# Kernel optimization log

Measured on AMD Instinct MI355X. Metric: run time of the kernel, lower is better.

Reference implementation:

```python
import jax, jax.numpy as jnp
import numpy as np

HEADS = 8


def setup_inputs() -> dict:
    key = jax.random.key(0)
    k1, k2, k3, k4, k5, k6 = jax.random.split(key, 6)
    B, S, E = 2, 2048, 512
    D = E // HEADS
    return {
        "values": jax.random.normal(k1, (B, S, E), dtype=jnp.float32),
        "keys": jax.random.normal(k2, (B, S, E), dtype=jnp.float32),
        "queries": jax.random.normal(k3, (B, S, E), dtype=jnp.float32),
        "mask": jax.random.randint(k4, (B, 1, 1, S), 0, 2, dtype=jnp.int32),
        "W_v": jax.random.normal(k5, (D, D), dtype=jnp.float32) * (1.0 / np.sqrt(D)),
        "W_o": jax.random.normal(k6, (E, E), dtype=jnp.float32) * (1.0 / np.sqrt(E)),
        "b_o": jnp.zeros((E,), dtype=jnp.float32),
    }


def reference(values, keys, queries, mask, W_v, W_o, b_o):
    B, S, E = queries.shape
    H = HEADS
    D = E // H
    # reshape to (b, s, h, d) and apply the SAME W_v linear to v, k, q
    # (faithful to the original, which calls self.values on all three)
    v = jnp.einsum('bshd,ed->bshe', values.reshape(B, -1, H, D), W_v)
    k = jnp.einsum('bshd,ed->bshe', keys.reshape(B, -1, H, D), W_v)
    q = jnp.einsum('bshd,ed->bshe', queries.reshape(B, -1, H, D), W_v)
    # unscaled attention scores (original has no 1/sqrt(d))
    energy = jnp.einsum('bqhd,bkhd->bhqk', q, k)  # (b, h, q, k)
    energy = jnp.where(mask == 0, -jnp.inf, energy)
    attn = jax.nn.softmax(energy, axis=3)
    out = jnp.einsum('bhqk,bkhd->bqhd', attn, v)  # (b, q, h, d)
    out = out.reshape(B, S, E)
    return out @ W_o.T + b_o
```

## Files before the change

kernel.cpp:

```cpp
#include <hip/hip_runtime.h>


#define B_ 2
#define S_ 2048
#define E_ 512
#define H_ 8
#define D_ 64

typedef unsigned short ushort_t;
typedef __attribute__((ext_vector_type(8))) short short8;
typedef __attribute__((ext_vector_type(8))) _Float16 half8;
typedef __attribute__((ext_vector_type(4))) float f32x4;

__device__ __forceinline__ ushort_t f2bs(float x) {
    union { float f; unsigned int u; } a; a.f = x;
    unsigned int u = a.u;
    u += 0x7fffu + ((u >> 16) & 1u);
    return (ushort_t)(u >> 16);
}
__device__ __forceinline__ float bs2f(ushort_t h) {
    union { unsigned int u; float f; } a; a.u = ((unsigned int)h) << 16;
    return a.f;
}
__device__ __forceinline__ ushort_t f2hs(float x) {
    _Float16 h = (_Float16)x;
    ushort_t u; __builtin_memcpy(&u, &h, 2);
    return u;
}
__device__ __forceinline__ void split16(const float4* g, ushort_t* hi, ushort_t* lo) {
    #pragma unroll
    for (int q = 0; q < 4; ++q) {
        float4 f = g[q];
        float vv[4] = {f.x, f.y, f.z, f.w};
        #pragma unroll
        for (int j = 0; j < 4; ++j) {
            ushort_t h = f2bs(vv[j]);
            hi[q * 4 + j] = h;
            lo[q * 4 + j] = f2bs(vv[j] - bs2f(h));
        }
    }
}

__global__ void __launch_bounds__(256) proj_mfma(
    const float* __restrict__ quer, const float* __restrict__ keys,
    const float* __restrict__ vals, const float* __restrict__ Wv,
    ushort_t* __restrict__ qf, ushort_t* __restrict__ kf,
    ushort_t* __restrict__ vt)
{
    __shared__ ushort_t Ah[64 * 72], Al[64 * 72];
    __shared__ ushort_t Bh[64 * 72], Bl[64 * 72];
    const int tens = blockIdx.y;
    const float* src = tens == 0 ? quer : (tens == 1 ? keys : vals);
    const int bx = blockIdx.x;
    const int st = bx & 31, bh = bx >> 5;
    const int b = bh >> 3, h = bh & 7;
    const int s0 = st * 64;
    const int t = threadIdx.x;

    {
        int e = t >> 2, dg = (t & 3) * 16;
        ushort_t th[16], tl[16];
        split16((const float4*)(Wv + e * 64 + dg), th, tl);
        *(uint4*)&Bh[e * 72 + dg] = *(uint4*)th;  *(uint4*)&Bh[e * 72 + dg + 8] = *(uint4*)(th + 8);
        *(uint4*)&Bl[e * 72 + dg] = *(uint4*)tl;  *(uint4*)&Bl[e * 72 + dg + 8] = *(uint4*)(tl + 8);
    }
    {
        int row = t >> 2, cg = (t & 3) * 16;
        const float* g = src + ((size_t)b * S_ + s0 + row) * 512 + h * 64 + cg;
        ushort_t th[16], tl[16];
        split16((const float4*)g, th, tl);
        *(uint4*)&Ah[row * 72 + cg] = *(uint4*)th;  *(uint4*)&Ah[row * 72 + cg + 8] = *(uint4*)(th + 8);
        *(uint4*)&Al[row * 72 + cg] = *(uint4*)tl;  *(uint4*)&Al[row * 72 + cg + 8] = *(uint4*)(tl + 8);
    }
    __syncthreads();

    const int w = t >> 6, lm = t & 15, quad = (t >> 4) & 3;
    f32x4 acc[4];
    #pragma unroll
    for (int nt = 0; nt < 4; ++nt) acc[nt] = (f32x4){0.f, 0.f, 0.f, 0.f};

    #pragma unroll
    for (int kk = 0; kk < 2; ++kk) {
        short8 ah = *(const short8*)&Ah[(w * 16 + lm) * 72 + kk * 32 + quad * 8];
        short8 al = *(const short8*)&Al[(w * 16 + lm) * 72 + kk * 32 + quad * 8];
        #pragma unroll
        for (int nt = 0; nt < 4; ++nt) {
            short8 bh8 = *(const short8*)&Bh[(nt * 16 + lm) * 72 + kk * 32 + quad * 8];
            short8 bl8 = *(const short8*)&Bl[(nt * 16 + lm) * 72 + kk * 32 + quad * 8];
            acc[nt] = __builtin_amdgcn_mfma_f32_16x16x32_bf16(ah, bh8, acc[nt], 0, 0, 0);
            acc[nt] = __builtin_amdgcn_mfma_f32_16x16x32_bf16(al, bh8, acc[nt], 0, 0, 0);
            acc[nt] = __builtin_amdgcn_mfma_f32_16x16x32_bf16(ah, bl8, acc[nt], 0, 0, 0);
        }
    }

    if (tens < 2) {
        ushort_t* dst = tens == 0 ? qf : kf;
        #pragma unroll
        for (int nt = 0; nt < 4; ++nt) {
            #pragma unroll
            for (int r = 0; r < 4; ++r) {
                size_t addr = ((size_t)bh * S_ + s0 + w * 16 + quad * 4 + r) * 64 + nt * 16 + lm;
                dst[addr] = f2hs(acc[nt][r]);
            }
        }
    } else {
        #pragma unroll
        for (int nt = 0; nt < 4; ++nt) {
            unsigned int p0 = (unsigned int)f2bs(acc[nt][0]) | ((unsigned int)f2bs(acc[nt][1]) << 16);
            unsigned int p1 = (unsigned int)f2bs(acc[nt][2]) | ((unsigned int)f2bs(acc[nt][3]) << 16);
            uint2 pk; pk.x = p0; pk.y = p1;
            size_t addr = ((size_t)bh * 64 + nt * 16 + lm) * S_ + s0 + w * 16 + quad * 4;
            *(uint2*)&vt[addr] = pk;
        }
    }
}

__global__ void __launch_bounds__(256) attn_mfma(
    const ushort_t* __restrict__ qf, const ushort_t* __restrict__ kf,
    const ushort_t* __restrict__ vt, const int* __restrict__ mask,
    ushort_t* __restrict__ ctx)
{
    __shared__ ushort_t Ks[64 * 72];
    __shared__ ushort_t Vt[64 * 72];
    __shared__ ushort_t Ps[4 * 16 * 72];
    __shared__ float    mbias[64];

    const int bx = blockIdx.x;
    const int qt = bx & 31;
    const int bh = bx >> 5;
    const int b  = bh >> 3, h = bh & 7;
    const int t  = threadIdx.x;
    const int w = t >> 6, lm = t & 15, quad = (t >> 4) & 3;
    const int q0 = qt * 64;
    const int wbase = w * 16 * 72;

    half8 aq[2];
    {
        size_t qrow = ((size_t)bh * S_ + q0 + w * 16 + lm) * 64 + quad * 8;
        #pragma unroll
        for (int kk = 0; kk < 2; ++kk)
            aq[kk] = *(const half8*)&qf[qrow + kk * 32];
    }
    short8 ones;
    #pragma unroll
    for (int j = 0; j < 8; ++j) ones[j] = (short)0x3F80;

    f32x4 acc[4];
    #pragma unroll
    for (int nt = 0; nt < 4; ++nt) acc[nt] = (f32x4){0.f, 0.f, 0.f, 0.f};
    f32x4 acc_l = (f32x4){0.f, 0.f, 0.f, 0.f};

    for (int kc = 0; kc < S_ / 64; ++kc) {
        __syncthreads();
        {
            int row = t >> 2, cg = (t & 3) * 16;
            size_t gaddr = ((size_t)bh * S_ + kc * 64 + row) * 64 + cg;
            *(uint4*)&Ks[row * 72 + cg]     = *(const uint4*)&kf[gaddr];
            *(uint4*)&Ks[row * 72 + cg + 8] = *(const uint4*)&kf[gaddr + 8];
        }
        {
            int row = t >> 2, cg = (t & 3) * 16;
            size_t gaddr = ((size_t)bh * 64 + row) * S_ + kc * 64 + cg;
            *(uint4*)&Vt[row * 72 + cg]     = *(const uint4*)&vt[gaddr];
            *(uint4*)&Vt[row * 72 + cg + 8] = *(const uint4*)&vt[gaddr + 8];
        }
        if (t < 64) mbias[t] = mask[b * S_ + kc * 64 + t] ? -64.f : -1e30f;
        __syncthreads();

        #pragma unroll
        for (int nt = 0; nt < 4; ++nt) {
            f32x4 s = (f32x4){0.f, 0.f, 0.f, 0.f};
            #pragma unroll
            for (int kk = 0; kk < 2; ++kk) {
                half8 bk = *(const half8*)&Ks[(nt * 16 + lm) * 72 + kk * 32 + quad * 8];
                s = __builtin_amdgcn_mfma_f32_16x16x32_f16(aq[kk], bk, s, 0, 0, 0);
            }
            float mv = mbias[nt * 16 + lm];
            #pragma unroll
            for (int r = 0; r < 4; ++r) {
                float p = __expf(s[r] + mv);
                Ps[wbase + (quad * 4 + r) * 72 + nt * 16 + lm] = f2bs(p);
            }
        }
        __builtin_amdgcn_s_waitcnt(0);

        #pragma unroll
        for (int kk = 0; kk < 2; ++kk) {
            short8 ap = *(const short8*)&Ps[wbase + lm * 72 + kk * 32 + quad * 8];
            #pragma unroll
            for (int nt = 0; nt < 4; ++nt) {
                short8 bv = *(const short8*)&Vt[(nt * 16 + lm) * 72 + kk * 32 + quad * 8];
                acc[nt] = __builtin_amdgcn_mfma_f32_16x16x32_bf16(ap, bv, acc[nt], 0, 0, 0);
            }
            acc_l = __builtin_amdgcn_mfma_f32_16x16x32_bf16(ap, ones, acc_l, 0, 0, 0);
        }
    }

    #pragma unroll
    for (int r = 0; r < 4; ++r) {
        float inv = 1.f / acc_l[r];
        int s = q0 + w * 16 + quad * 4 + r;
        #pragma unroll
        for (int nt = 0; nt < 4; ++nt) {
            int d = nt * 16 + lm;
            ctx[((size_t)b * S_ + s) * E_ + h * D_ + d] = f2bs(acc[nt][r] * inv);
        }
    }
}

__global__ void __launch_bounds__(256) outproj_mfma(
    const ushort_t* __restrict__ ctx, const float* __restrict__ Wo,
    const float* __restrict__ bo, float* __restrict__ out)
{
    __shared__ ushort_t As[64 * 72];
    __shared__ ushort_t Bs[64 * 72];
    const int m0 = blockIdx.x * 64, n0 = blockIdx.y * 64;
    const int t = threadIdx.x;
    const int w = t >> 6, lm = t & 15, quad = (t >> 4) & 3;

    f32x4 acc[4];
    #pragma unroll
    for (int nt = 0; nt < 4; ++nt) acc[nt] = (f32x4){0.f, 0.f, 0.f, 0.f};

    for (int kc = 0; kc < E_ / 64; ++kc) {
        __syncthreads();
        {
            int row = t >> 2, cg = (t & 3) * 16;
            const ushort_t* g = ctx + (size_t)(m0 + row) * E_ + kc * 64 + cg;
            *(uint4*)&As[row * 72 + cg]     = *(const uint4*)g;
            *(uint4*)&As[row * 72 + cg + 8] = *(const uint4*)(g + 8);
        }
        {
            int n = t >> 2, kg = (t & 3) * 16;
            const float4* g = (const float4*)(Wo + (size_t)(n0 + n) * E_ + kc * 64 + kg);
            ushort_t tmp[16];
            #pragma unroll
            for (int q = 0; q < 4; ++q) {
                float4 f = g[q];
                tmp[q * 4 + 0] = f2bs(f.x); tmp[q * 4 + 1] = f2bs(f.y);
                tmp[q * 4 + 2] = f2bs(f.z); tmp[q * 4 + 3] = f2bs(f.w);
            }
            *(uint4*)&Bs[n * 72 + kg]     = *(uint4*)tmp;
            *(uint4*)&Bs[n * 72 + kg + 8] = *(uint4*)(tmp + 8);
        }
        __syncthreads();

        #pragma unroll
        for (int kk = 0; kk < 2; ++kk) {
            short8 a = *(const short8*)&As[(w * 16 + lm) * 72 + kk * 32 + quad * 8];
            #pragma unroll
            for (int nt = 0; nt < 4; ++nt) {
                short8 bb = *(const short8*)&Bs[(nt * 16 + lm) * 72 + kk * 32 + quad * 8];
                acc[nt] = __builtin_amdgcn_mfma_f32_16x16x32_bf16(a, bb, acc[nt], 0, 0, 0);
            }
        }
    }

    #pragma unroll
    for (int nt = 0; nt < 4; ++nt) {
        float bias = bo[n0 + nt * 16 + lm];
        #pragma unroll
        for (int r = 0; r < 4; ++r) {
            int m = m0 + w * 16 + quad * 4 + r;
            out[(size_t)m * E_ + n0 + nt * 16 + lm] = acc[nt][r] + bias;
        }
    }
}

extern "C" void kernel_launch(void* const* d_in, const int* in_sizes, int n_in,
                              void* d_out, int out_size, void* d_ws, size_t ws_size,
                              hipStream_t stream) {
    const float* vals = (const float*)d_in[0];
    const float* keys = (const float*)d_in[1];
    const float* quer = (const float*)d_in[2];
    const int*   mask = (const int*)d_in[3];
    const float* Wv   = (const float*)d_in[4];
    const float* Wo   = (const float*)d_in[5];
    const float* bo   = (const float*)d_in[6];
    float* out = (float*)d_out;

    const size_t N = (size_t)B_ * H_ * S_ * D_;
    ushort_t* ws  = (ushort_t*)d_ws;
    ushort_t* qf  = ws;
    ushort_t* kf  = ws + N;
    ushort_t* vt  = ws + 2 * N;
    ushort_t* ctx = ws + 3 * N;

    proj_mfma<<<dim3(B_ * H_ * (S_ / 64), 3), 256, 0, stream>>>(
        quer, keys, vals, Wv, qf, kf, vt);
    attn_mfma<<<B_ * H_ * (S_ / 64), 256, 0, stream>>>(qf, kf, vt, mask, ctx);
    outproj_mfma<<<dim3((B_ * S_) / 64, E_ / 64), 256, 0, stream>>>(ctx, Wo, bo, out);
}
```

Baseline: 147.8 us.

## Rewrite pipeline with weight prep kernel, register-resident tiles and split-K attention

Adds a prep kernel that converts Wo to bf16 and splits Wv into hi/lo bf16 once per call. Projection and output-projection kernels drop shared-memory staging and read operands straight from global into registers, one 16-row tile per wave. Attention now uses 128-thread blocks of 32 queries, where each of two waves covers half the keys, prefetches the next K/V chunk into registers, and loads mask values directly. The two partial sums are merged through shared memory. This removes per-chunk block barriers and adds occupancy, at the cost of redundant global loads, more registers per thread and an extra launch.

Result: slower. 185.1 us (+25.2%).

```diff
diff --git a/kernel.cpp b/kernel.cpp
--- a/kernel.cpp
+++ b/kernel.cpp
@@ -27,232 +27,254 @@
     ushort_t u; __builtin_memcpy(&u, &h, 2);
     return u;
 }
-__device__ __forceinline__ void split16(const float4* g, ushort_t* hi, ushort_t* lo) {
-    #pragma unroll
-    for (int q = 0; q < 4; ++q) {
-        float4 f = g[q];
-        float vv[4] = {f.x, f.y, f.z, f.w};
-        #pragma unroll
-        for (int j = 0; j < 4; ++j) {
-            ushort_t h = f2bs(vv[j]);
-            hi[q * 4 + j] = h;
-            lo[q * 4 + j] = f2bs(vv[j] - bs2f(h));
-        }
+
+__global__ void __launch_bounds__(256) prep_kernel(
+    const float* __restrict__ Wv, const float* __restrict__ Wo,
+    ushort_t* __restrict__ wvh, ushort_t* __restrict__ wvl,
+    ushort_t* __restrict__ wob)
+{
+    const int t = threadIdx.x;
+    size_t base = ((size_t)blockIdx.x * 256 + t) * 4;
+    float4 f = *(const float4*)&Wo[base];
+    ushort_t o4[4] = {f2bs(f.x), f2bs(f.y), f2bs(f.z), f2bs(f.w)};
+    *(uint2*)&wob[base] = *(uint2*)o4;
+    if (blockIdx.x == 0) {
+        ushort_t hi[16], lo[16];
+        #pragma unroll
+        for (int q = 0; q < 4; ++q) {
+            float4 g = *(const float4*)&Wv[t * 16 + q * 4];
+            float vv[4] = {g.x, g.y, g.z, g.w};
+            #pragma unroll
+            for (int j = 0; j < 4; ++j) {
+                ushort_t h = f2bs(vv[j]);
+                hi[q * 4 + j] = h;
+                lo[q * 4 + j] = f2bs(vv[j] - bs2f(h));
+            }
+        }
+        *(uint4*)&wvh[t * 16]     = *(uint4*)hi;
+        *(uint4*)&wvh[t * 16 + 8] = *(uint4*)(hi + 8);
+        *(uint4*)&wvl[t * 16]     = *(uint4*)lo;
+        *(uint4*)&wvl[t * 16 + 8] = *(uint4*)(lo + 8);
     }
 }
 
 __global__ void __launch_bounds__(256) proj_mfma(
     const float* __restrict__ quer, const float* __restrict__ keys,
-    const float* __restrict__ vals, const float* __restrict__ Wv,
-    ushort_t* __restrict__ qf, ushort_t* __restrict__ kf,
-    ushort_t* __restrict__ vt)
+    const float* __restrict__ vals,
+    const ushort_t* __restrict__ wvh, const ushort_t* __restrict__ wvl,
+    ushort_t* __restrict__ qf, ushort_t* __restrict__ kf, ushort_t* __restrict__ vt)
 {
-    __shared__ ushort_t Ah[64 * 72], Al[64 * 72];
-    __shared__ ushort_t Bh[64 * 72], Bl[64 * 72];
-    const int tens = blockIdx.y;
+    const int t   = threadIdx.x;
+    const int wid = blockIdx.x * 4 + (t >> 6);
+    const int tens = wid >> 11;
+    const int rem  = wid & 2047;
+    const int bh = rem >> 7, st = rem & 127;
+    const int s0 = st * 16;
+    const int b = bh >> 3, h = bh & 7;
+    const int lm = t & 15, quad = (t >> 4) & 3;
     const float* src = tens == 0 ? quer : (tens == 1 ? keys : vals);
-    const int bx = blockIdx.x;
-    const int st = bx & 31, bh = bx >> 5;
-    const int b = bh >> 3, h = bh & 7;
-    const int s0 = st * 64;
-    const int t = threadIdx.x;
-
-    {
-        int e = t >> 2, dg = (t & 3) * 16;
-        ushort_t th[16], tl[16];
-        split16((const float4*)(Wv + e * 64 + dg), th, tl);
-        *(uint4*)&Bh[e * 72 + dg] = *(uint4*)th;  *(uint4*)&Bh[e * 72 + dg + 8] = *(uint4*)(th + 8);
-        *(uint4*)&Bl[e * 72 + dg] = *(uint4*)tl;  *(uint4*)&Bl[e * 72 + dg + 8] = *(uint4*)(tl + 8);
-    }
-    {
-        int row = t >> 2, cg = (t & 3) * 16;
-        const float* g = src + ((size_t)b * S_ + s0 + row) * 512 + h * 64 + cg;
-        ushort_t th[16], tl[16];
-        split16((const float4*)g, th, tl);
-        *(uint4*)&Ah[row * 72 + cg] = *(uint4*)th;  *(uint4*)&Ah[row * 72 + cg + 8] = *(uint4*)(th + 8);
-        *(uint4*)&Al[row * 72 + cg] = *(uint4*)tl;  *(uint4*)&Al[row * 72 + cg + 8] = *(uint4*)(tl + 8);
-    }
-    __syncthreads();
-
-    const int w = t >> 6, lm = t & 15, quad = (t >> 4) & 3;
+
+    short8 ah[2], al[2];
+    #pragma unroll
+    for (int kk = 0; kk < 2; ++kk) {
+        const float* g = src + ((size_t)b * S_ + s0 + lm) * E_ + h * 64 + kk * 32 + quad * 8;
+        float4 x0 = *(const float4*)g;
+        float4 x1 = *(const float4*)(g + 4);
+        float xv[8] = {x0.x, x0.y, x0.z, x0.w, x1.x, x1.y, x1.z, x1.w};
+        #pragma unroll
+        for (int j = 0; j < 8; ++j) {
+            ushort_t hi = f2bs(xv[j]);
+            ah[kk][j] = (short)hi;
+            al[kk][j] = (short)f2bs(xv[j] - bs2f(hi));
+        }
+    }
+
     f32x4 acc[4];
     #pragma unroll
     for (int nt = 0; nt < 4; ++nt) acc[nt] = (f32x4){0.f, 0.f, 0.f, 0.f};
 
     #pragma unroll
     for (int kk = 0; kk < 2; ++kk) {
-        short8 ah = *(const short8*)&Ah[(w * 16 + lm) * 72 + kk * 32 + quad * 8];
-        short8 al = *(const short8*)&Al[(w * 16 + lm) * 72 + kk * 32 + quad * 8];
         #pragma unroll
         for (int nt = 0; nt < 4; ++nt) {
-            short8 bh8 = *(const short8*)&Bh[(nt * 16 + lm) * 72 + kk * 32 + quad * 8];
-            short8 bl8 = *(const short8*)&Bl[(nt * 16 + lm) * 72 + kk * 32 + quad * 8];
-            acc[nt] = __builtin_amdgcn_mfma_f32_16x16x32_bf16(ah, bh8, acc[nt], 0, 0, 0);
-            acc[nt] = __builtin_amdgcn_mfma_f32_16x16x32_bf16(al, bh8, acc[nt], 0, 0, 0);
-            acc[nt] = __builtin_amdgcn_mfma_f32_16x16x32_bf16(ah, bl8, acc[nt], 0, 0, 0);
+            size_t wad = (size_t)(nt * 16 + lm) * 64 + kk * 32 + quad * 8;
+            short8 bh8 = *(const short8*)&wvh[wad];
+            short8 bl8 = *(const short8*)&wvl[wad];
+            acc[nt] = __builtin_amdgcn_mfma_f32_16x16x32_bf16(ah[kk], bh8, acc[nt], 0, 0, 0);
+            acc[nt] = __builtin_amdgcn_mfma_f32_16x16x32_bf16(al[kk], bh8, acc[nt], 0, 0, 0);
+            acc[nt] = __builtin_amdgcn_mfma_f32_16x16x32_bf16(ah[kk], bl8, acc[nt], 0, 0, 0);
         }
     }
 
     if (tens < 2) {
         ushort_t* dst = tens == 0 ? qf : kf;
         #pragma unroll
+        for (int nt = 0; nt < 4; ++nt)
+            #pragma unroll
+            for (int r = 0; r < 4; ++r)
+                dst[((size_t)bh * S_ + s0 + quad * 4 + r) * 64 + nt * 16 + lm] = f2hs(acc[nt][r]);
+    } else {
+        #pragma unroll
         for (int nt = 0; nt < 4; ++nt) {
-            #pragma unroll
-            for (int r = 0; r < 4; ++r) {
-                size_t addr = ((size_t)bh * S_ + s0 + w * 16 + quad * 4 + r) * 64 + nt * 16 + lm;
-                dst[addr] = f2hs(acc[nt][r]);
-            }
-        }
-    } else {
-        #pragma unroll
-        for (int nt = 0; nt < 4; ++nt) {
-            unsigned int p0 = (unsigned int)f2bs(acc[nt][0]) | ((unsigned int)f2bs(acc[nt][1]) << 16);
-            unsigned int p1 = (unsigned int)f2bs(acc[nt][2]) | ((unsigned int)f2bs(acc[nt][3]) << 16);
-            uint2 pk; pk.x = p0; pk.y = p1;
-            size_t addr = ((size_t)bh * 64 + nt * 16 + lm) * S_ + s0 + w * 16 + quad * 4;
-            *(uint2*)&vt[addr] = pk;
-        }
-    }
-}
-
-__global__ void __launch_bounds__(256) attn_mfma(
+            ushort_t p4[4] = {f2bs(acc[nt][0]), f2bs(acc[nt][1]), f2bs(acc[nt][2]), f2bs(acc[nt][3])};
+            *(uint2*)&vt[((size_t)bh * 64 + nt * 16 + lm) * S_ + s0 + quad * 4] = *(uint2*)p4;
+        }
+    }
+}
+
+__global__ void __launch_bounds__(128) attn_mfma(
     const ushort_t* __restrict__ qf, const ushort_t* __restrict__ kf,
     const ushort_t* __restrict__ vt, const int* __restrict__ mask,
     ushort_t* __restrict__ ctx)
 {
-    __shared__ ushort_t Ks[64 * 72];
-    __shared__ ushort_t Vt[64 * 72];
-    __shared__ ushort_t Ps[4 * 16 * 72];
-    __shared__ float    mbias[64];
-
-    const int bx = blockIdx.x;
-    const int qt = bx & 31;
-    const int bh = bx >> 5;
-    const int b  = bh >> 3, h = bh & 7;
-    const int t  = threadIdx.x;
-    const int w = t >> 6, lm = t & 15, quad = (t >> 4) & 3;
-    const int q0 = qt * 64;
-    const int wbase = w * 16 * 72;
-
-    half8 aq[2];
-    {
-        size_t qrow = ((size_t)bh * S_ + q0 + w * 16 + lm) * 64 + quad * 8;
+    __shared__ ushort_t Ps[2][32 * 72];
+    __shared__ float    cbuf[32 * 68];
+    const int t = threadIdx.x;
+    const int w = t >> 6;
+    const int lm = t & 15, quad = (t >> 4) & 3;
+    const int x = blockIdx.x;
+    const int bh = (x & 7) * 2 + ((x >> 3) & 1);
+    const int qt = x >> 4;
+    const int qw0 = qt * 32;
+    const int b = bh >> 3, h = bh & 7;
+
+    half8 aq[2][2];
+    #pragma unroll
+    for (int u = 0; u < 2; ++u)
         #pragma unroll
         for (int kk = 0; kk < 2; ++kk)
-            aq[kk] = *(const half8*)&qf[qrow + kk * 32];
-    }
+            aq[u][kk] = *(const half8*)&qf[((size_t)bh * S_ + qw0 + u * 16 + lm) * 64 + kk * 32 + quad * 8];
+
     short8 ones;
     #pragma unroll
     for (int j = 0; j < 8; ++j) ones[j] = (short)0x3F80;
 
-    f32x4 acc[4];
-    #pragma unroll
-    for (int nt = 0; nt < 4; ++nt) acc[nt] = (f32x4){0.f, 0.f, 0.f, 0.f};
-    f32x4 acc_l = (f32x4){0.f, 0.f, 0.f, 0.f};
-
-    for (int kc = 0; kc < S_ / 64; ++kc) {
-        __syncthreads();
-        {
-            int row = t >> 2, cg = (t & 3) * 16;
-            size_t gaddr = ((size_t)bh * S_ + kc * 64 + row) * 64 + cg;
-            *(uint4*)&Ks[row * 72 + cg]     = *(const uint4*)&kf[gaddr];
-            *(uint4*)&Ks[row * 72 + cg + 8] = *(const uint4*)&kf[gaddr + 8];
-        }
-        {
-            int row = t >> 2, cg = (t & 3) * 16;
-            size_t gaddr = ((size_t)bh * 64 + row) * S_ + kc * 64 + cg;
-            *(uint4*)&Vt[row * 72 + cg]     = *(const uint4*)&vt[gaddr];
-            *(uint4*)&Vt[row * 72 + cg + 8] = *(const uint4*)&vt[gaddr + 8];
-        }
-        if (t < 64) mbias[t] = mask[b * S_ + kc * 64 + t] ? -64.f : -1e30f;
-        __syncthreads();
-
-        #pragma unroll
-        for (int nt = 0; nt < 4; ++nt) {
-            f32x4 s = (f32x4){0.f, 0.f, 0.f, 0.f};
+    half8 kb[8]; short8 vb[8];
+    auto load_k = [&](int kc) {
+        #pragma unroll
+        for (int mt = 0; mt < 4; ++mt)
+            #pragma unroll
+            for (int kk = 0; kk < 2; ++kk)
+                kb[mt * 2 + kk] = *(const half8*)&kf[((size_t)bh * S_ + kc * 64 + mt * 16 + lm) * 64 + kk * 32 + quad * 8];
+    };
+    auto load_v = [&](int kc) {
+        #pragma unroll
+        for (int nt = 0; nt < 4; ++nt)
+            #pragma unroll
+            for (int kk = 0; kk < 2; ++kk)
+                vb[nt * 2 + kk] = *(const short8*)&vt[((size_t)bh * 64 + nt * 16 + lm) * S_ + kc * 64 + kk * 32 + quad * 8];
+    };
+
+    const int kc0 = w * 16;
+    load_k(kc0);
+    load_v(kc0);
+
+    f32x4 acc[2][4];
+    #pragma unroll
+    for (int u = 0; u < 2; ++u)
+        #pragma unroll
+        for (int nt = 0; nt < 4; ++nt) acc[u][nt] = (f32x4){0.f, 0.f, 0.f, 0.f};
+    f32x4 accl[2] = {(f32x4){0.f, 0.f, 0.f, 0.f}, (f32x4){0.f, 0.f, 0.f, 0.f}};
+
+    for (int i = 0; i < 16; ++i) {
+        const int kc = kc0 + i;
+        float mv[4][4];
+        #pragma unroll
+        for (int mt = 0; mt < 4; ++mt) {
+            int4 mi = *(const int4*)&mask[b * S_ + kc * 64 + mt * 16 + quad * 4];
+            mv[mt][0] = mi.x ? -64.f : -1e30f;
+            mv[mt][1] = mi.y ? -64.f : -1e30f;
+            mv[mt][2] = mi.z ? -64.f : -1e30f;
+            mv[mt][3] = mi.w ? -64.f : -1e30f;
+        }
+        f32x4 stt[2][4];
+        #pragma unroll
+        for (int u = 0; u < 2; ++u)
+            #pragma unroll
+            for (int mt = 0; mt < 4; ++mt) {
+                f32x4 s = (f32x4){0.f, 0.f, 0.f, 0.f};
+                s = __builtin_amdgcn_mfma_f32_16x16x32_f16(kb[mt * 2 + 0], aq[u][0], s, 0, 0, 0);
+                s = __builtin_amdgcn_mfma_f32_16x16x32_f16(kb[mt * 2 + 1], aq[u][1], s, 0, 0, 0);
+                stt[u][mt] = s;
+            }
+        const int kcn = (i < 15) ? kc + 1 : kc0;
+        load_k(kcn);
+
+        #pragma unroll
+        for (int u = 0; u < 2; ++u)
+            #pragma unroll
+            for (int mt = 0; mt < 4; ++mt) {
+                ushort_t p4[4];
+                #pragma unroll
+                for (int r = 0; r < 4; ++r)
+                    p4[r] = f2bs(__expf(stt[u][mt][r] + mv[mt][r]));
+                *(uint2*)&Ps[w][u * 1152 + lm * 72 + mt * 16 + quad * 4] = *(uint2*)p4;
+            }
+        #pragma unroll
+        for (int u = 0; u < 2; ++u)
             #pragma unroll
             for (int kk = 0; kk < 2; ++kk) {
-                half8 bk = *(const half8*)&Ks[(nt * 16 + lm) * 72 + kk * 32 + quad * 8];
-                s = __builtin_amdgcn_mfma_f32_16x16x32_f16(aq[kk], bk, s, 0, 0, 0);
-            }
-            float mv = mbias[nt * 16 + lm];
+                short8 ap = *(const short8*)&Ps[w][u * 1152 + lm * 72 + kk * 32 + quad * 8];
+                #pragma unroll
+                for (int nt = 0; nt < 4; ++nt)
+                    acc[u][nt] = __builtin_amdgcn_mfma_f32_16x16x32_bf16(ap, vb[nt * 2 + kk], acc[u][nt], 0, 0, 0);
+                accl[u] = __builtin_amdgcn_mfma_f32_16x16x32_bf16(ap, ones, accl[u], 0, 0, 0);
+            }
+        load_v(kcn);
+    }
+
+    if (w == 1) {
+        #pragma unroll
+        for (int u = 0; u < 2; ++u) {
             #pragma unroll
             for (int r = 0; r < 4; ++r) {
-                float p = __expf(s[r] + mv);
-                Ps[wbase + (quad * 4 + r) * 72 + nt * 16 + lm] = f2bs(p);
-            }
-        }
-        __builtin_amdgcn_s_waitcnt(0);
-
-        #pragma unroll
-        for (int kk = 0; kk < 2; ++kk) {
-            short8 ap = *(const short8*)&Ps[wbase + lm * 72 + kk * 32 + quad * 8];
-            #pragma unroll
-            for (int nt = 0; nt < 4; ++nt) {
-                short8 bv = *(const short8*)&Vt[(nt * 16 + lm) * 72 + kk * 32 + quad * 8];
-                acc[nt] = __builtin_amdgcn_mfma_f32_16x16x32_bf16(ap, bv, acc[nt], 0, 0, 0);
-            }
-            acc_l = __builtin_amdgcn_mfma_f32_16x16x32_bf16(ap, ones, acc_l, 0, 0, 0);
-        }
-    }
-
-    #pragma unroll
-    for (int r = 0; r < 4; ++r) {
-        float inv = 1.f / acc_l[r];
-        int s = q0 + w * 16 + quad * 4 + r;
-        #pragma unroll
-        for (int nt = 0; nt < 4; ++nt) {
-            int d = nt * 16 + lm;
-            ctx[((size_t)b * S_ + s) * E_ + h * D_ + d] = f2bs(acc[nt][r] * inv);
+                int q = u * 16 + quad * 4 + r;
+                #pragma unroll
+                for (int nt = 0; nt < 4; ++nt)
+                    cbuf[q * 68 + nt * 16 + lm] = acc[u][nt][r];
+                cbuf[q * 68 + 64] = accl[u][r];
+            }
+        }
+    }
+    __syncthreads();
+    if (w == 0) {
+        #pragma unroll
+        for (int u = 0; u < 2; ++u) {
+            #pragma unroll
+            for (int r = 0; r < 4; ++r) {
+                int q = u * 16 + quad * 4 + r;
+                float l = accl[u][r] + cbuf[q * 68 + 64];
+                float inv = 1.f / l;
+                int qg = qw0 + q;
+                #pragma unroll
+                for (int nt = 0; nt < 4; ++nt) {
+                    float o = acc[u][nt][r] + cbuf[q * 68 + nt * 16 + lm];
+                    ctx[((size_t)b * S_ + qg) * E_ + h * D_ + nt * 16 + lm] = f2bs(o * inv);
+                }
+            }
         }
     }
 }
 
 __global__ void __launch_bounds__(256) outproj_mfma(
-    const ushort_t* __restrict__ ctx, const float* __restrict__ Wo,
+    const ushort_t* __restrict__ ctx, const ushort_t* __restrict__ wob,
     const float* __restrict__ bo, float* __restrict__ out)
 {
-    __shared__ ushort_t As[64 * 72];
-    __shared__ ushort_t Bs[64 * 72];
-    const int m0 = blockIdx.x * 64, n0 = blockIdx.y * 64;
     const int t = threadIdx.x;
-    const int w = t >> 6, lm = t & 15, quad = (t >> 4) & 3;
+    const int wid = blockIdx.x * 4 + (t >> 6);
+    const int m0 = (wid >> 3) * 16, n0 = (wid & 7) * 64;
+    const int lm = t & 15, quad = (t >> 4) & 3;
 
     f32x4 acc[4];
     #pragma unroll
     for (int nt = 0; nt < 4; ++nt) acc[nt] = (f32x4){0.f, 0.f, 0.f, 0.f};
 
-    for (int kc = 0; kc < E_ / 64; ++kc) {
-        __syncthreads();
-        {
-            int row = t >> 2, cg = (t & 3) * 16;
-            const ushort_t* g = ctx + (size_t)(m0 + row) * E_ + kc * 64 + cg;
-            *(uint4*)&As[row * 72 + cg]     = *(const uint4*)g;
-            *(uint4*)&As[row * 72 + cg + 8] = *(const uint4*)(g + 8);
-        }
-        {
-            int n = t >> 2, kg = (t & 3) * 16;
-            const float4* g = (const float4*)(Wo + (size_t)(n0 + n) * E_ + kc * 64 + kg);
-            ushort_t tmp[16];
-            #pragma unroll
-            for (int q = 0; q < 4; ++q) {
-                float4 f = g[q];
-                tmp[q * 4 + 0] = f2bs(f.x); tmp[q * 4 + 1] = f2bs(f.y);
-                tmp[q * 4 + 2] = f2bs(f.z); tmp[q * 4 + 3] = f2bs(f.w);
-            }
-            *(uint4*)&Bs[n * 72 + kg]     = *(uint4*)tmp;
-            *(uint4*)&Bs[n * 72 + kg + 8] = *(uint4*)(tmp + 8);
-        }
-        __syncthreads();
-
-        #pragma unroll
-        for (int kk = 0; kk < 2; ++kk) {
-            short8 a = *(const short8*)&As[(w * 16 + lm) * 72 + kk * 32 + quad * 8];
-            #pragma unroll
-            for (int nt = 0; nt < 4; ++nt) {
-                short8 bb = *(const short8*)&Bs[(nt * 16 + lm) * 72 + kk * 32 + quad * 8];
-                acc[nt] = __builtin_amdgcn_mfma_f32_16x16x32_bf16(a, bb, acc[nt], 0, 0, 0);
-            }
+    for (int ks = 0; ks < 16; ++ks) {
+        short8 a = *(const short8*)&ctx[(size_t)(m0 + lm) * E_ + ks * 32 + quad * 8];
+        #pragma unroll
+        for (int nt = 0; nt < 4; ++nt) {
+            short8 bb = *(const short8*)&wob[(size_t)(n0 + nt * 16 + lm) * E_ + ks * 32 + quad * 8];
+            acc[nt] = __builtin_amdgcn_mfma_f32_16x16x32_bf16(a, bb, acc[nt], 0, 0, 0);
         }
     }
 
@@ -260,10 +282,8 @@
     for (int nt = 0; nt < 4; ++nt) {
         float bias = bo[n0 + nt * 16 + lm];
         #pragma unroll
-        for (int r = 0; r < 4; ++r) {
-            int m = m0 + w * 16 + quad * 4 + r;
-            out[(size_t)m * E_ + n0 + nt * 16 + lm] = acc[nt][r] + bias;
-        }
+        for (int r = 0; r < 4; ++r)
+            out[(size_t)(m0 + quad * 4 + r) * E_ + n0 + nt * 16 + lm] = acc[nt][r] + bias;
     }
 }
 
@@ -285,9 +305,12 @@
     ushort_t* kf  = ws + N;
     ushort_t* vt  = ws + 2 * N;
     ushort_t* ctx = ws + 3 * N;
-
-    proj_mfma<<<dim3(B_ * H_ * (S_ / 64), 3), 256, 0, stream>>>(
-        quer, keys, vals, Wv, qf, kf, vt);
-    attn_mfma<<<B_ * H_ * (S_ / 64), 256, 0, stream>>>(qf, kf, vt, mask, ctx);
-    outproj_mfma<<<dim3((B_ * S_) / 64, E_ / 64), 256, 0, stream>>>(ctx, Wo, bo, out);
-}
+    ushort_t* wvh = ws + 4 * N;
+    ushort_t* wvl = wvh + 4096;
+    ushort_t* wob = wvl + 4096;
+
+    prep_kernel<<<256, 256, 0, stream>>>(Wv, Wo, wvh, wvl, wob);
+    proj_mfma<<<1536, 256, 0, stream>>>(quer, keys, vals, wvh, wvl, qf, kf, vt);
+    attn_mfma<<<1024, 128, 0, stream>>>(qf, kf, vt, mask, ctx);
+    outproj_mfma<<<512, 256, 0, stream>>>(ctx, wob, bo, out);
+}
```
